# Kernel tuning notes

Measured on AMD Instinct MI355X. Metric: run time of the kernel, lower is better.

Reference implementation:

```python
import jax, jax.numpy as jnp
import numpy as np

B, CO, P = 4, 80, 9          # batch, out_channels, point_num
HI, WI = 128, 128            # input feature-map size
HO, WO = 128, 128            # output (location) spatial size


def setup_inputs() -> dict:
    key = jax.random.key(0)
    k1, k2, k3 = jax.random.split(key, 3)
    x = jax.random.normal(k1, (B, P * CO, HI, WI), jnp.float32)
    # location holds absolute (y, x) coords, interleaved per point: 2*P channels
    loc = jax.random.uniform(k2, (B, 2 * P, HO, WO), jnp.float32) * (HI - 1)
    bias = jax.random.normal(k3, (CO,), jnp.float32) * 0.01
    return {"x": x, "location": loc, "bias": bias}


def _collect_merge(x, location, bias):
    Bn, Cin, Hi, Wi = x.shape
    Pn = location.shape[1] // 2
    Ho, Wo = location.shape[2], location.shape[3]
    Co = Cin // Pn  # channels_offset == out_channels
    feat = x.reshape(Bn, Pn, Co, Hi * Wi)           # [B,P,Co,Hi*Wi]
    loc = location.reshape(Bn, Pn, 2, Ho, Wo)
    y, xc = loc[:, :, 0], loc[:, :, 1]              # [B,P,Ho,Wo]
    y0 = jnp.floor(y)
    x0 = jnp.floor(xc)
    dy, dx = y - y0, xc - x0
    y0i = y0.astype(jnp.int32)
    x0i = x0.astype(jnp.int32)
    out = jnp.zeros((Bn, Pn, Co, Ho * Wo), x.dtype)
    taps = [(0, 0, (1 - dy) * (1 - dx)), (0, 1, (1 - dy) * dx),
            (1, 0, dy * (1 - dx)), (1, 1, dy * dx)]
    for oy, ox, w in taps:  # 4 bilinear taps (fixed small loop)
        yi = y0i + oy
        xi = x0i + ox
        valid = (yi >= 0) & (yi < Hi) & (xi >= 0) & (xi < Wi)
        idx = (jnp.clip(yi, 0, Hi - 1) * Wi + jnp.clip(xi, 0, Wi - 1))
        idx = idx.reshape(Bn, Pn, 1, Ho * Wo)
        tap = jnp.take_along_axis(
            feat, jnp.broadcast_to(idx, (Bn, Pn, Co, Ho * Wo)), axis=3)
        out = out + tap * (w * valid).reshape(Bn, Pn, 1, Ho * Wo)
    # merge (sum over point_num) + per-channel bias
    out = out.sum(axis=1).reshape(Bn, Co, Ho, Wo) + bias[None, :, None, None]
    return out


def reference(x, location, bias):
    return _collect_merge(x, location, bias)
```

## Files before the change

### kernel.cpp

```cpp
#include <hip/hip_runtime.h>
#include <cstddef>
#include <cstdint>

constexpr int B_  = 4;
constexpr int CO_ = 80;
constexpr int PN_ = 9;
constexpr int HI_ = 128;
constexpr int WI_ = 128;
constexpr int HW_ = HI_ * WI_;

__device__ __forceinline__ uint16_t f2bf(float f) {
    uint32_t u = __float_as_uint(f);
    return (uint16_t)((u + 0x7fffu + ((u >> 16) & 1u)) >> 16);
}

__global__ __launch_bounds__(256) void transpose_bf16_k(const float* __restrict__ x,
                                                        uint16_t* __restrict__ xt) {
    const int bp  = blockIdx.y;
    const int hw0 = blockIdx.x << 7;

    __shared__ uint16_t tile[CO_][136];

    const float* src = x + (size_t)bp * CO_ * HW_ + hw0;
    for (int i = threadIdx.x; i < CO_ * 32; i += 256) {
        const int co = i >> 5;
        const int h4 = (i & 31) << 2;
        const float4 v = *(const float4*)(src + (size_t)co * HW_ + h4);
        ushort4 pk;
        pk.x = f2bf(v.x); pk.y = f2bf(v.y); pk.z = f2bf(v.z); pk.w = f2bf(v.w);
        *(ushort4*)&tile[co][h4] = pk;
    }
    __syncthreads();

    uint32_t* dst = (uint32_t*)(xt + ((size_t)bp * HW_ + hw0) * CO_);
    for (int i = threadIdx.x; i < 128 * 10; i += 256) {
        const int px = i / 10;
        const int cp = i - px * 10;
        uint4 wv;
        uint32_t* w = (uint32_t*)&wv;
#pragma unroll
        for (int j = 0; j < 4; ++j) {
            const uint32_t lo = tile[cp * 8 + 2 * j][px];
            const uint32_t hi = tile[cp * 8 + 2 * j + 1][px];
            w[j] = lo | (hi << 16);
        }
        *(uint4*)(dst + px * 40 + cp * 4) = wv;
    }
}

__global__ __launch_bounds__(320) void gather_bf16_k(const uint16_t* __restrict__ xt,
                                                     const float* __restrict__ loc,
                                                     const float* __restrict__ bias,
                                                     float* __restrict__ out) {
    const int b   = blockIdx.x >> 8;
    const int hw0 = (blockIdx.x & 255) << 6;
    const int tid = threadIdx.x;

    __shared__ union SM {
        struct { float w[PN_][64][4]; int off[PN_][64][4]; } ab;
        float accs[64][81];
    } sm;

    for (int item = tid; item < PN_ * 64; item += 320) {
        const int p    = item >> 6;
        const int pixl = item & 63;
        const float y = loc[(((size_t)b * PN_ + p) * 2 + 0) * HW_ + hw0 + pixl];
        const float x = loc[(((size_t)b * PN_ + p) * 2 + 1) * HW_ + hw0 + pixl];
        const float y0f = floorf(y), x0f = floorf(x);
        const int   y0 = (int)y0f,  x0 = (int)x0f;
        const float dy = y - y0f,   dx = x - x0f;
        const float w[4] = { (1.f - dy) * (1.f - dx), (1.f - dy) * dx,
                             dy * (1.f - dx),         dy * dx };
#pragma unroll
        for (int c = 0; c < 4; ++c) {
            const int yi = y0 + (c >> 1);
            const int xi = x0 + (c & 1);
            const bool valid = (yi >= 0) & (yi < HI_) & (xi >= 0) & (xi < WI_);
            const int yc = min(max(yi, 0), HI_ - 1);
            const int xc = min(max(xi, 0), WI_ - 1);
            sm.ab.w[p][pixl][c]   = valid ? w[c] : 0.f;
            sm.ab.off[p][pixl][c] = (yc * WI_ + xc) * (CO_ * 2);
        }
    }
    __syncthreads();

    const int px0 = tid / 10;
    const int cg  = tid - px0 * 10;
    const int px1 = px0 + 32;

    float acc0[8], acc1[8];
#pragma unroll
    for (int j = 0; j < 8; ++j) { acc0[j] = bias[cg * 8 + j]; acc1[j] = acc0[j]; }

    for (int p = 0; p < PN_; ++p) {
        const char* base = (const char*)(xt + ((size_t)b * PN_ + p) * (size_t)HW_ * CO_)
                           + cg * 16;
        uint4 v0[4], v1[4];
        float w0[4], w1[4];
#pragma unroll
        for (int c = 0; c < 4; ++c) {
            v0[c] = *(const uint4*)(base + sm.ab.off[p][px0][c]);
            w0[c] = sm.ab.w[p][px0][c];
        }
#pragma unroll
        for (int c = 0; c < 4; ++c) {
            v1[c] = *(const uint4*)(base + sm.ab.off[p][px1][c]);
            w1[c] = sm.ab.w[p][px1][c];
        }
#pragma unroll
        for (int c = 0; c < 4; ++c) {
            const uint32_t* u0 = (const uint32_t*)&v0[c];
            const uint32_t* u1 = (const uint32_t*)&v1[c];
#pragma unroll
            for (int j = 0; j < 4; ++j) {
                acc0[2*j]   = fmaf(__uint_as_float(u0[j] << 16),        w0[c], acc0[2*j]);
                acc0[2*j+1] = fmaf(__uint_as_float(u0[j] & 0xffff0000u), w0[c], acc0[2*j+1]);
                acc1[2*j]   = fmaf(__uint_as_float(u1[j] << 16),        w1[c], acc1[2*j]);
                acc1[2*j+1] = fmaf(__uint_as_float(u1[j] & 0xffff0000u), w1[c], acc1[2*j+1]);
            }
        }
    }

    __syncthreads();
#pragma unroll
    for (int j = 0; j < 8; ++j) {
        sm.accs[px0][cg * 8 + j] = acc0[j];
        sm.accs[px1][cg * 8 + j] = acc1[j];
    }
    __syncthreads();

    for (int i = tid; i < 64 * CO_; i += 320) {
        const int co  = i >> 6;
        const int hwl = i & 63;
        out[((size_t)b * CO_ + co) * HW_ + hw0 + hwl] = sm.accs[hwl][co];
    }
}

__global__ __launch_bounds__(256) void gather_direct_k(const float* __restrict__ xsrc,
                                                       const float* __restrict__ loc,
                                                       const float* __restrict__ bias,
                                                       float* __restrict__ out) {
    const int b   = blockIdx.x >> 10;
    const int hw0 = (blockIdx.x & 1023) << 4;
    const int tid = threadIdx.x;

    __shared__ float wts[PN_][16][4];
    __shared__ int   idxs[PN_][16][4];
    __shared__ float accs[16][CO_ + 1];

    if (tid < PN_ * 16) {
        const int p    = tid >> 4;
        const int pixl = tid & 15;
        const float y = loc[(((size_t)b * PN_ + p) * 2 + 0) * HW_ + hw0 + pixl];
        const float x = loc[(((size_t)b * PN_ + p) * 2 + 1) * HW_ + hw0 + pixl];
        const float y0f = floorf(y), x0f = floorf(x);
        const int   y0 = (int)y0f,  x0 = (int)x0f;
        const float dy = y - y0f,   dx = x - x0f;
        const float w[4] = { (1.f - dy) * (1.f - dx), (1.f - dy) * dx,
                             dy * (1.f - dx),         dy * dx };
#pragma unroll
        for (int c = 0; c < 4; ++c) {
            const int yi = y0 + (c >> 1);
            const int xi = x0 + (c & 1);
            const bool valid = (yi >= 0) & (yi < HI_) & (xi >= 0) & (xi < WI_);
            const int yc = min(max(yi, 0), HI_ - 1);
            const int xc = min(max(xi, 0), WI_ - 1);
            wts[p][pixl][c]  = valid ? w[c] : 0.f;
            idxs[p][pixl][c] = yc * WI_ + xc;
        }
    }
    __syncthreads();

    float myacc[5];
    int   cos[5], pixls[5];
#pragma unroll
    for (int k = 0; k < 5; ++k) {
        const int item = tid + (k << 8);
        const int pixl = item / CO_;
        const int co   = item - pixl * CO_;
        cos[k] = co; pixls[k] = pixl;
        myacc[k] = bias[co];
    }
    for (int p = 0; p < PN_; ++p) {
        const float* base = xsrc + ((size_t)b * PN_ + p) * CO_ * HW_;
#pragma unroll
        for (int k = 0; k < 5; ++k) {
#pragma unroll
            for (int c = 0; c < 4; ++c) {
                const int   idx = idxs[p][pixls[k]][c];
                const float w   = wts[p][pixls[k]][c];
                myacc[k] = fmaf(base[(size_t)cos[k] * HW_ + idx], w, myacc[k]);
            }
        }
    }
#pragma unroll
    for (int k = 0; k < 5; ++k) accs[pixls[k]][cos[k]] = myacc[k];
    __syncthreads();
    for (int i = tid; i < 16 * CO_; i += 256) {
        const int co  = i >> 4;
        const int hwl = i & 15;
        out[((size_t)b * CO_ + co) * HW_ + hw0 + hwl] = accs[hwl][co];
    }
}

extern "C" void kernel_launch(void* const* d_in, const int* in_sizes, int n_in,
                              void* d_out, int out_size, void* d_ws, size_t ws_size,
                              hipStream_t stream) {
    const float* x    = (const float*)d_in[0];
    const float* loc  = (const float*)d_in[1];
    const float* bias = (const float*)d_in[2];
    float*       out  = (float*)d_out;

    const size_t need = (size_t)B_ * PN_ * CO_ * HW_ * sizeof(uint16_t);
    if (ws_size >= need) {
        uint16_t* xt = (uint16_t*)d_ws;
        dim3 g1(HW_ / 128, B_ * PN_);
        transpose_bf16_k<<<g1, 256, 0, stream>>>(x, xt);
        gather_bf16_k<<<dim3(B_ * HW_ / 64), 320, 0, stream>>>(xt, loc, bias, out);
    } else {
        gather_direct_k<<<dim3(B_ * HW_ / 16), 256, 0, stream>>>(x, loc, bias, out);
    }
}
```

Measured before the change: 115.8 us.

## Pipeline per-batch transpose with previous batch's gather in fused launches

Replaces the two-kernel transpose-then-gather with a per-batch sequence of fused launches. Each launch transposes batch i to bf16 channel-last while other blocks gather batch i-1, interleaving the two block types 9:2. It also pads the channel stride to 96 when workspace allows, and halves the gather tile to 32 pixels per block with one pixel per thread. The aim is to overlap the bandwidth-bound transpose with the latency-bound gather and improve gather alignment. The cost is more launches, smaller tiles, and a larger workspace footprint.

```diff
diff --git a/kernel.cpp b/kernel.cpp
--- a/kernel.cpp
+++ b/kernel.cpp
@@ -9,61 +9,68 @@
 constexpr int WI_ = 128;
 constexpr int HW_ = HI_ * WI_;
 
+constexpr int NTHR   = 320;
+constexpr int THW    = 64;
+constexpr int TUNITS = PN_ * (HW_ / THW);
+constexpr int GPX    = 32;
+constexpr int GUNITS = HW_ / GPX;
+
+union SMU {
+    struct { float w[PN_][GPX][4]; int off[PN_][GPX][4]; } ab;
+    float    accs[GPX][81];
+    uint16_t tile[CO_][72];
+};
+
 __device__ __forceinline__ uint16_t f2bf(float f) {
     uint32_t u = __float_as_uint(f);
     return (uint16_t)((u + 0x7fffu + ((u >> 16) & 1u)) >> 16);
 }
 
-__global__ __launch_bounds__(256) void transpose_bf16_k(const float* __restrict__ x,
-                                                        uint16_t* __restrict__ xt) {
-    const int bp  = blockIdx.y;
-    const int hw0 = blockIdx.x << 7;
-
-    __shared__ uint16_t tile[CO_][136];
-
-    const float* src = x + (size_t)bp * CO_ * HW_ + hw0;
-    for (int i = threadIdx.x; i < CO_ * 32; i += 256) {
-        const int co = i >> 5;
-        const int h4 = (i & 31) << 2;
+template <int COP>
+__device__ __forceinline__ void t_unit(const float* __restrict__ x,
+                                       uint16_t* __restrict__ xt,
+                                       int b, int u, SMU* sm, int tid) {
+    const int p   = u >> 8;
+    const int hw0 = (u & 255) << 6;
+    const size_t plane = (size_t)(b * PN_ + p);
+
+    const float* src = x + plane * CO_ * (size_t)HW_ + hw0;
+    for (int i = tid; i < CO_ * (THW / 4); i += NTHR) {
+        const int co = i >> 4;
+        const int h4 = (i & 15) << 2;
         const float4 v = *(const float4*)(src + (size_t)co * HW_ + h4);
         ushort4 pk;
         pk.x = f2bf(v.x); pk.y = f2bf(v.y); pk.z = f2bf(v.z); pk.w = f2bf(v.w);
-        *(ushort4*)&tile[co][h4] = pk;
-    }
-    __syncthreads();
-
-    uint32_t* dst = (uint32_t*)(xt + ((size_t)bp * HW_ + hw0) * CO_);
-    for (int i = threadIdx.x; i < 128 * 10; i += 256) {
+        *(ushort4*)&sm->tile[co][h4] = pk;
+    }
+    __syncthreads();
+    uint16_t* dst = xt + (plane * HW_ + hw0) * COP;
+    for (int i = tid; i < THW * (CO_ / 8); i += NTHR) {
         const int px = i / 10;
         const int cp = i - px * 10;
         uint4 wv;
         uint32_t* w = (uint32_t*)&wv;
 #pragma unroll
         for (int j = 0; j < 4; ++j) {
-            const uint32_t lo = tile[cp * 8 + 2 * j][px];
-            const uint32_t hi = tile[cp * 8 + 2 * j + 1][px];
+            const uint32_t lo = sm->tile[cp * 8 + 2 * j][px];
+            const uint32_t hi = sm->tile[cp * 8 + 2 * j + 1][px];
             w[j] = lo | (hi << 16);
         }
-        *(uint4*)(dst + px * 40 + cp * 4) = wv;
-    }
-}
-
-__global__ __launch_bounds__(320) void gather_bf16_k(const uint16_t* __restrict__ xt,
-                                                     const float* __restrict__ loc,
-                                                     const float* __restrict__ bias,
-                                                     float* __restrict__ out) {
-    const int b   = blockIdx.x >> 8;
-    const int hw0 = (blockIdx.x & 255) << 6;
-    const int tid = threadIdx.x;
-
-    __shared__ union SM {
-        struct { float w[PN_][64][4]; int off[PN_][64][4]; } ab;
-        float accs[64][81];
-    } sm;
-
-    for (int item = tid; item < PN_ * 64; item += 320) {
-        const int p    = item >> 6;
-        const int pixl = item & 63;
+        *(uint4*)(dst + px * COP + cp * 8) = wv;
+    }
+}
+
+template <int COP>
+__device__ __forceinline__ void g_unit(const uint16_t* __restrict__ xt,
+                                       const float* __restrict__ loc,
+                                       const float* __restrict__ bias,
+                                       float* __restrict__ out,
+                                       int b, int u, SMU* sm, int tid) {
+    const int hw0 = u * GPX;
+
+    if (tid < PN_ * GPX) {
+        const int p    = tid >> 5;
+        const int pixl = tid & 31;
         const float y = loc[(((size_t)b * PN_ + p) * 2 + 0) * HW_ + hw0 + pixl];
         const float x = loc[(((size_t)b * PN_ + p) * 2 + 1) * HW_ + hw0 + pixl];
         const float y0f = floorf(y), x0f = floorf(x);
@@ -78,62 +85,67 @@
             const bool valid = (yi >= 0) & (yi < HI_) & (xi >= 0) & (xi < WI_);
             const int yc = min(max(yi, 0), HI_ - 1);
             const int xc = min(max(xi, 0), WI_ - 1);
-            sm.ab.w[p][pixl][c]   = valid ? w[c] : 0.f;
-            sm.ab.off[p][pixl][c] = (yc * WI_ + xc) * (CO_ * 2);
-        }
-    }
-    __syncthreads();
-
-    const int px0 = tid / 10;
-    const int cg  = tid - px0 * 10;
-    const int px1 = px0 + 32;
-
-    float acc0[8], acc1[8];
-#pragma unroll
-    for (int j = 0; j < 8; ++j) { acc0[j] = bias[cg * 8 + j]; acc1[j] = acc0[j]; }
+            sm->ab.w[p][pixl][c]   = valid ? w[c] : 0.f;
+            sm->ab.off[p][pixl][c] = (yc * WI_ + xc) * (COP * 2);
+        }
+    }
+    __syncthreads();
+
+    const int px = tid / 10;
+    const int cg = tid - px * 10;
+
+    float acc[8];
+#pragma unroll
+    for (int j = 0; j < 8; ++j) acc[j] = bias[cg * 8 + j];
 
     for (int p = 0; p < PN_; ++p) {
-        const char* base = (const char*)(xt + ((size_t)b * PN_ + p) * (size_t)HW_ * CO_)
+        const char* base = (const char*)(xt + ((size_t)b * PN_ + p) * (size_t)HW_ * COP)
                            + cg * 16;
-        uint4 v0[4], v1[4];
-        float w0[4], w1[4];
-#pragma unroll
-        for (int c = 0; c < 4; ++c) {
-            v0[c] = *(const uint4*)(base + sm.ab.off[p][px0][c]);
-            w0[c] = sm.ab.w[p][px0][c];
-        }
-#pragma unroll
-        for (int c = 0; c < 4; ++c) {
-            v1[c] = *(const uint4*)(base + sm.ab.off[p][px1][c]);
-            w1[c] = sm.ab.w[p][px1][c];
-        }
-#pragma unroll
-        for (int c = 0; c < 4; ++c) {
-            const uint32_t* u0 = (const uint32_t*)&v0[c];
-            const uint32_t* u1 = (const uint32_t*)&v1[c];
+        uint4 v[4]; float w[4];
+#pragma unroll
+        for (int c = 0; c < 4; ++c) {
+            v[c] = *(const uint4*)(base + sm->ab.off[p][px][c]);
+            w[c] = sm->ab.w[p][px][c];
+        }
+#pragma unroll
+        for (int c = 0; c < 4; ++c) {
+            const uint32_t* uu = (const uint32_t*)&v[c];
 #pragma unroll
             for (int j = 0; j < 4; ++j) {
-                acc0[2*j]   = fmaf(__uint_as_float(u0[j] << 16),        w0[c], acc0[2*j]);
-                acc0[2*j+1] = fmaf(__uint_as_float(u0[j] & 0xffff0000u), w0[c], acc0[2*j+1]);
-                acc1[2*j]   = fmaf(__uint_as_float(u1[j] << 16),        w1[c], acc1[2*j]);
-                acc1[2*j+1] = fmaf(__uint_as_float(u1[j] & 0xffff0000u), w1[c], acc1[2*j+1]);
+                acc[2*j]   = fmaf(__uint_as_float(uu[j] << 16),         w[c], acc[2*j]);
+                acc[2*j+1] = fmaf(__uint_as_float(uu[j] & 0xffff0000u), w[c], acc[2*j+1]);
             }
         }
     }
-
-    __syncthreads();
-#pragma unroll
-    for (int j = 0; j < 8; ++j) {
-        sm.accs[px0][cg * 8 + j] = acc0[j];
-        sm.accs[px1][cg * 8 + j] = acc1[j];
-    }
-    __syncthreads();
-
-    for (int i = tid; i < 64 * CO_; i += 320) {
-        const int co  = i >> 6;
-        const int hwl = i & 63;
-        out[((size_t)b * CO_ + co) * HW_ + hw0 + hwl] = sm.accs[hwl][co];
-    }
+    __syncthreads();
+#pragma unroll
+    for (int j = 0; j < 8; ++j) sm->accs[px][cg * 8 + j] = acc[j];
+    __syncthreads();
+
+    for (int i = tid; i < GPX * CO_; i += NTHR) {
+        const int co  = i >> 5;
+        const int hwl = i & 31;
+        out[((size_t)b * CO_ + co) * HW_ + hw0 + hwl] = sm->accs[hwl][co];
+    }
+}
+
+template <int COP>
+__global__ __launch_bounds__(NTHR) void pipe_k(const float* __restrict__ x,
+                                               const float* __restrict__ loc,
+                                               const float* __restrict__ bias,
+                                               float* __restrict__ out,
+                                               uint16_t* __restrict__ xt,
+                                               int tb, int gb) {
+    __shared__ SMU sm;
+    const int bid = blockIdx.x;
+    const int tid = threadIdx.x;
+
+    if (gb < 0) { t_unit<COP>(x, xt, tb, bid, &sm, tid); return; }
+    if (tb < 0) { g_unit<COP>(xt, loc, bias, out, gb, bid, &sm, tid); return; }
+    const int grp = bid / 11;
+    const int r   = bid - grp * 11;
+    if (r < 2) g_unit<COP>(xt, loc, bias, out, gb, grp * 2 + r, &sm, tid);
+    else       t_unit<COP>(x, xt, tb, grp * 9 + (r - 2), &sm, tid);
 }
 
 __global__ __launch_bounds__(256) void gather_direct_k(const float* __restrict__ xsrc,
@@ -182,7 +194,7 @@
         myacc[k] = bias[co];
     }
     for (int p = 0; p < PN_; ++p) {
-        const float* base = xsrc + ((size_t)b * PN_ + p) * CO_ * HW_;
+        const float* base = xsrc + ((size_t)b * PN_ + p) * CO_ * (size_t)HW_;
 #pragma unroll
         for (int k = 0; k < 5; ++k) {
 #pragma unroll
@@ -201,6 +213,15 @@
         const int hwl = i & 15;
         out[((size_t)b * CO_ + co) * HW_ + hw0 + hwl] = accs[hwl][co];
     }
+}
+
+template <int COP>
+static void launch_pipeline(const float* x, const float* loc, const float* bias,
+                            float* out, uint16_t* xt, hipStream_t stream) {
+    pipe_k<COP><<<dim3(TUNITS), NTHR, 0, stream>>>(x, loc, bias, out, xt, 0, -1);
+    for (int i = 1; i < B_; ++i)
+        pipe_k<COP><<<dim3(TUNITS + GUNITS), NTHR, 0, stream>>>(x, loc, bias, out, xt, i, i - 1);
+    pipe_k<COP><<<dim3(GUNITS), NTHR, 0, stream>>>(x, loc, bias, out, xt, -1, B_ - 1);
 }
 
 extern "C" void kernel_launch(void* const* d_in, const int* in_sizes, int n_in,
@@ -211,12 +232,13 @@
     const float* bias = (const float*)d_in[2];
     float*       out  = (float*)d_out;
 
-    const size_t need = (size_t)B_ * PN_ * CO_ * HW_ * sizeof(uint16_t);
-    if (ws_size >= need) {
-        uint16_t* xt = (uint16_t*)d_ws;
-        dim3 g1(HW_ / 128, B_ * PN_);
-        transpose_bf16_k<<<g1, 256, 0, stream>>>(x, xt);
-        gather_bf16_k<<<dim3(B_ * HW_ / 64), 320, 0, stream>>>(xt, loc, bias, out);
+    const size_t need96 = (size_t)B_ * PN_ * HW_ * 96 * sizeof(uint16_t);
+    const size_t need80 = (size_t)B_ * PN_ * HW_ * 80 * sizeof(uint16_t);
+
+    if (ws_size >= need96) {
+        launch_pipeline<96>(x, loc, bias, out, (uint16_t*)d_ws, stream);
+    } else if (ws_size >= need80) {
+        launch_pipeline<80>(x, loc, bias, out, (uint16_t*)d_ws, stream);
     } else {
         gather_direct_k<<<dim3(B_ * HW_ / 16), 256, 0, stream>>>(x, loc, bias, out);
     }
```

Result: slower. 207.5 us (+79.1%).
